# Kernel optimization log

Hardware: AMD Instinct MI355X
Metric: run time of the kernel (lower is better)

## Reference

```python
import jax, jax.numpy as jnp
import numpy as np

XI = 10.0
LAMBDA_SCALE = 1e-4
NUM_CLASSES = 13
KNOWN_NUM_CLASSES = 12  # all labels except 'unknown'
EPS = 1e-10
B, D = 262144, 512


def setup_inputs() -> dict:
    key = jax.random.key(0)
    k1, k2, k3, k4, k5 = jax.random.split(key, 5)
    logits = jax.random.normal(k1, (B, NUM_CLASSES), dtype=jnp.float32)
    true_y = jax.random.randint(k2, (B,), 0, NUM_CLASSES, dtype=jnp.int64)
    is_unknown = jax.random.randint(k3, (B,), 0, 2, dtype=jnp.int32).astype(bool)
    deep_features = jax.random.normal(k4, (B, D), dtype=jnp.float32)
    weights = jax.random.uniform(k5, (NUM_CLASSES,), dtype=jnp.float32, minval=0.5, maxval=2.0)
    return {"logits": logits, "true_y": true_y, "is_unknown": is_unknown,
            "deep_features": deep_features, "weights": weights}


def reference(logits, true_y, is_unknown, deep_features, weights):
    # softmax over classes, then log(softmax + eps) as in the original
    sm = jax.nn.softmax(logits, axis=1)                      # [B, C]
    log_sm = jnp.log(sm + EPS)                               # [B, C]
    feat_mag = jnp.linalg.norm(deep_features, axis=1)        # [B]

    # unknown branch: uniform log-loss over all classes + squared-magnitude penalty
    je_unknown = -(1.0 / KNOWN_NUM_CLASSES) * jnp.sum(log_sm, axis=1)
    pen_unknown = feat_mag ** 2
    jr_unknown = je_unknown + LAMBDA_SCALE * pen_unknown

    # known branch: NLL of true class + hinge-squared magnitude penalty
    je_known = -jnp.take_along_axis(log_sm, true_y[:, None], axis=1)[:, 0]
    pen_known = jnp.maximum(XI - feat_mag, 0.0) ** 2
    jr_known = je_known + LAMBDA_SCALE * pen_known

    jr = jnp.where(is_unknown, jr_unknown, jr_known)         # [B]
    w = weights[true_y]                                      # [B]
    loss = jnp.sum(w * jr) / jnp.sum(w)
    return loss
```

## Files before the change

kernel.cpp:

```cpp
#include <hip/hip_runtime.h>
#include <math.h>


typedef float f32x4 __attribute__((ext_vector_type(4)));

constexpr int   CLS  = 13;
constexpr float INV_KNOWN = 1.0f / 12.0f;
constexpr float LAM  = 1e-4f;
constexpr float XI   = 10.0f;

constexpr int BLOCK = 256;
constexpr int WPB   = BLOCK / 64;

template<int CTRL, int RMASK>
__device__ __forceinline__ float dpp_add(float v) {
    int t = __builtin_amdgcn_update_dpp(0, __builtin_bit_cast(int, v),
                                        CTRL, RMASK, 0xF, true);
    return v + __builtin_bit_cast(float, t);
}
__device__ __forceinline__ float read_lane_f(float v, int lane) {
    return __builtin_bit_cast(float,
        __builtin_amdgcn_readlane(__builtin_bit_cast(int, v), lane));
}

__global__ __launch_bounds__(256) void obj_main(
    const float*  __restrict__ logits,
    const int*    __restrict__ true_y,
    const int*    __restrict__ is_unknown,
    const f32x4*  __restrict__ feat,
    const float*  __restrict__ weights,
    double*       __restrict__ partials,
    int B)
{
    const int lane = threadIdx.x & 63;
    const int wid  = threadIdx.x >> 6;
    const int gw   = blockIdx.x * WPB + wid;
    const int tw   = gridDim.x * WPB;

    double num = 0.0, den = 0.0;

    int row = gw;
    f32x4 a = (f32x4)0.0f, b = (f32x4)0.0f;
    float x = 0.0f;
    if (row < B) {
        const f32x4* fr = feat + (size_t)row * 128;
        a = fr[lane];
        b = fr[lane + 64];
        if (lane < CLS) x = logits[(size_t)row * CLS + lane];
    }

    while (row < B) {
        const int nrow = row + tw;
        f32x4 na = (f32x4)0.0f, nb = (f32x4)0.0f;
        float nx = 0.0f;
        if (nrow < B) {
            const f32x4* fr = feat + (size_t)nrow * 128;
            na = fr[lane];
            nb = fr[lane + 64];
            if (lane < CLS) nx = logits[(size_t)nrow * CLS + lane];
        }

        float ss = fmaf(a.x, a.x, fmaf(a.y, a.y, fmaf(a.z, a.z, a.w * a.w)))
                 + fmaf(b.x, b.x, fmaf(b.y, b.y, fmaf(b.z, b.z, b.w * b.w)));
        const float e = (lane < CLS) ? __expf(x) : 0.0f;
        float S = e, sx = x;

        ss = dpp_add<0x111, 0xF>(ss);
        S  = dpp_add<0x111, 0xF>(S);
        sx = dpp_add<0x111, 0xF>(sx);
        ss = dpp_add<0x112, 0xF>(ss);
        S  = dpp_add<0x112, 0xF>(S);
        sx = dpp_add<0x112, 0xF>(sx);
        ss = dpp_add<0x114, 0xF>(ss);
        S  = dpp_add<0x114, 0xF>(S);
        sx = dpp_add<0x114, 0xF>(sx);
        ss = dpp_add<0x118, 0xF>(ss);
        S  = dpp_add<0x118, 0xF>(S);
        sx = dpp_add<0x118, 0xF>(sx);
        ss = dpp_add<0x142, 0xA>(ss);
        ss = dpp_add<0x143, 0xC>(ss);

        const int   ty    = true_y[row];
        const int   unk   = is_unknown[row];
        const float w     = weights[ty];
        const float ss_t  = read_lane_f(ss, 63);
        const float S_t   = read_lane_f(S,  15);
        const float sx_t  = read_lane_f(sx, 15);
        const float x_ty  = read_lane_f(x,  ty);
        const float logS  = __logf(S_t);
        const float mag   = sqrtf(ss_t);

        const float jr_u = fmaf(LAM, ss_t, -INV_KNOWN * (sx_t - (float)CLS * logS));
        const float dk   = fmaxf(XI - mag, 0.0f);
        const float jr_k = fmaf(LAM, dk * dk, logS - x_ty);
        const float jr   = unk ? jr_u : jr_k;

        num += (double)(w * jr);
        den += (double)w;

        row = nrow; a = na; b = nb; x = nx;
    }

    __shared__ double s_num[WPB], s_den[WPB];
    if (lane == 0) { s_num[wid] = num; s_den[wid] = den; }
    __syncthreads();
    if (threadIdx.x == 0) {
        double n = 0.0, d = 0.0;
        for (int i = 0; i < WPB; ++i) { n += s_num[i]; d += s_den[i]; }
        partials[blockIdx.x] = n;
        partials[gridDim.x + blockIdx.x] = d;
    }
}

__global__ __launch_bounds__(256) void obj_final(
    const double* __restrict__ partials, int nparts, float* __restrict__ out)
{
    const int lane = threadIdx.x & 63;
    const int wid  = threadIdx.x >> 6;
    double n = 0.0, d = 0.0;
    for (int i = threadIdx.x; i < nparts; i += blockDim.x) {
        n += partials[i];
        d += partials[nparts + i];
    }
    #pragma unroll
    for (int o = 32; o; o >>= 1) {
        n += __shfl_xor(n, o, 64);
        d += __shfl_xor(d, o, 64);
    }
    __shared__ double s_n[4], s_d[4];
    if (lane == 0) { s_n[wid] = n; s_d[wid] = d; }
    __syncthreads();
    if (threadIdx.x == 0) {
        double tn = 0.0, td = 0.0;
        for (int i = 0; i < 4; ++i) { tn += s_n[i]; td += s_d[i]; }
        out[0] = (float)(tn / td);
    }
}

extern "C" void kernel_launch(void* const* d_in, const int* in_sizes, int n_in,
                              void* d_out, int out_size, void* d_ws, size_t ws_size,
                              hipStream_t stream)
{
    const float*  logits     = (const float*)d_in[0];
    const int*    true_y     = (const int*)d_in[1];
    const int*    is_unknown = (const int*)d_in[2];
    const f32x4*  feat       = (const f32x4*)d_in[3];
    const float*  weights    = (const float*)d_in[4];
    float*        out        = (float*)d_out;
    const int B = in_sizes[1];

    double* partials = (double*)d_ws;
    constexpr int GRID = 2048;

    obj_main<<<GRID, BLOCK, 0, stream>>>(logits, true_y, is_unknown, feat,
                                         weights, partials, B);
    obj_final<<<1, 256, 0, stream>>>(partials, GRID, out);
}
```

Before: 101.7 us.

## Split softmax-NLL and feature-norm work into separate block groups

```diff
diff --git a/kernel.cpp b/kernel.cpp
--- a/kernel.cpp
+++ b/kernel.cpp
@@ -11,6 +11,8 @@
 
 constexpr int BLOCK = 256;
 constexpr int WPB   = BLOCK / 64;
+constexpr int NB_B  = 128;
+constexpr int NB_A  = 1920;
 
 template<int CTRL, int RMASK>
 __device__ __forceinline__ float dpp_add(float v) {
@@ -34,94 +36,116 @@
 {
     const int lane = threadIdx.x & 63;
     const int wid  = threadIdx.x >> 6;
-    const int gw   = blockIdx.x * WPB + wid;
-    const int tw   = gridDim.x * WPB;
 
-    double num = 0.0, den = 0.0;
+    if (blockIdx.x < NB_B) {
+        const int gwb = blockIdx.x * WPB + wid;
+        double numB = 0.0;
+        for (int it = 0; it < 8; ++it) {
+            const int r = (((gwb << 3) + it) << 6) | lane;
+            const float* lp = logits + (size_t)r * CLS;
+            float xv[CLS];
+            #pragma unroll
+            for (int c = 0; c < CLS; ++c) xv[c] = lp[c];
+            const int   ty  = true_y[r];
+            const int   unk = is_unknown[r];
+            const float w   = weights[ty];
 
-    int row = gw;
-    f32x4 a = (f32x4)0.0f, b = (f32x4)0.0f;
-    float x = 0.0f;
-    if (row < B) {
-        const f32x4* fr = feat + (size_t)row * 128;
-        a = fr[lane];
-        b = fr[lane + 64];
-        if (lane < CLS) x = logits[(size_t)row * CLS + lane];
-    }
+            float S = 0.0f, sx = 0.0f;
+            #pragma unroll
+            for (int c = 0; c < CLS; ++c) {
+                S  += __expf(xv[c]);
+                sx += xv[c];
+            }
+            const float logS = __logf(S);
+            float x_ty = xv[0];
+            #pragma unroll
+            for (int c = 1; c < CLS; ++c) x_ty = (ty == c) ? xv[c] : x_ty;
 
-    while (row < B) {
-        const int nrow = row + tw;
-        f32x4 na = (f32x4)0.0f, nb = (f32x4)0.0f;
-        float nx = 0.0f;
-        if (nrow < B) {
-            const f32x4* fr = feat + (size_t)nrow * 128;
-            na = fr[lane];
-            nb = fr[lane + 64];
-            if (lane < CLS) nx = logits[(size_t)nrow * CLS + lane];
+            const float je = unk ? (-INV_KNOWN * (sx - (float)CLS * logS))
+                                 : (logS - x_ty);
+            numB += (double)(w * je);
+        }
+        #pragma unroll
+        for (int o = 32; o; o >>= 1) numB += __shfl_xor(numB, o, 64);
+        __shared__ double s_b[WPB];
+        if (lane == 0) s_b[wid] = numB;
+        __syncthreads();
+        if (threadIdx.x == 0) {
+            double n = 0.0;
+            for (int i = 0; i < WPB; ++i) n += s_b[i];
+            partials[2 * NB_A + blockIdx.x] = n;
+        }
+    } else {
+        const int bidA = blockIdx.x - NB_B;
+        const int gw   = bidA * WPB + wid;
+        const int tw   = NB_A * WPB;
+
+        const float wreg = weights[lane < CLS ? lane : 0];
+
+        double num = 0.0, den = 0.0;
+        int row = gw;
+        f32x4 a = (f32x4)0.0f, b = (f32x4)0.0f;
+        if (row < B) {
+            const f32x4* fr = feat + (size_t)row * 128;
+            a = fr[lane];
+            b = fr[lane + 64];
         }
 
-        float ss = fmaf(a.x, a.x, fmaf(a.y, a.y, fmaf(a.z, a.z, a.w * a.w)))
-                 + fmaf(b.x, b.x, fmaf(b.y, b.y, fmaf(b.z, b.z, b.w * b.w)));
-        const float e = (lane < CLS) ? __expf(x) : 0.0f;
-        float S = e, sx = x;
+        while (row < B) {
+            const int nrow = row + tw;
+            f32x4 na = (f32x4)0.0f, nb = (f32x4)0.0f;
+            if (nrow < B) {
+                const f32x4* fr = feat + (size_t)nrow * 128;
+                na = fr[lane];
+                nb = fr[lane + 64];
+            }
 
-        ss = dpp_add<0x111, 0xF>(ss);
-        S  = dpp_add<0x111, 0xF>(S);
-        sx = dpp_add<0x111, 0xF>(sx);
-        ss = dpp_add<0x112, 0xF>(ss);
-        S  = dpp_add<0x112, 0xF>(S);
-        sx = dpp_add<0x112, 0xF>(sx);
-        ss = dpp_add<0x114, 0xF>(ss);
-        S  = dpp_add<0x114, 0xF>(S);
-        sx = dpp_add<0x114, 0xF>(sx);
-        ss = dpp_add<0x118, 0xF>(ss);
-        S  = dpp_add<0x118, 0xF>(S);
-        sx = dpp_add<0x118, 0xF>(sx);
-        ss = dpp_add<0x142, 0xA>(ss);
-        ss = dpp_add<0x143, 0xC>(ss);
+            float ss = fmaf(a.x, a.x, fmaf(a.y, a.y, fmaf(a.z, a.z, a.w * a.w)))
+                     + fmaf(b.x, b.x, fmaf(b.y, b.y, fmaf(b.z, b.z, b.w * b.w)));
+            ss = dpp_add<0x111, 0xF>(ss);
+            ss = dpp_add<0x112, 0xF>(ss);
+            ss = dpp_add<0x114, 0xF>(ss);
+            ss = dpp_add<0x118, 0xF>(ss);
+            ss = dpp_add<0x142, 0xA>(ss);
+            ss = dpp_add<0x143, 0xC>(ss);
 
-        const int   ty    = true_y[row];
-        const int   unk   = is_unknown[row];
-        const float w     = weights[ty];
-        const float ss_t  = read_lane_f(ss, 63);
-        const float S_t   = read_lane_f(S,  15);
-        const float sx_t  = read_lane_f(sx, 15);
-        const float x_ty  = read_lane_f(x,  ty);
-        const float logS  = __logf(S_t);
-        const float mag   = sqrtf(ss_t);
+            const int   ty   = true_y[row];
+            const int   unk  = is_unknown[row];
+            const float w    = read_lane_f(wreg, ty);
+            const float ss_t = read_lane_f(ss, 63);
+            const float mag  = sqrtf(ss_t);
+            const float dk   = fmaxf(XI - mag, 0.0f);
+            const float pen  = unk ? ss_t : dk * dk;
 
-        const float jr_u = fmaf(LAM, ss_t, -INV_KNOWN * (sx_t - (float)CLS * logS));
-        const float dk   = fmaxf(XI - mag, 0.0f);
-        const float jr_k = fmaf(LAM, dk * dk, logS - x_ty);
-        const float jr   = unk ? jr_u : jr_k;
+            num += (double)(w * (LAM * pen));
+            den += (double)w;
 
-        num += (double)(w * jr);
-        den += (double)w;
+            row = nrow; a = na; b = nb;
+        }
 
-        row = nrow; a = na; b = nb; x = nx;
-    }
-
-    __shared__ double s_num[WPB], s_den[WPB];
-    if (lane == 0) { s_num[wid] = num; s_den[wid] = den; }
-    __syncthreads();
-    if (threadIdx.x == 0) {
-        double n = 0.0, d = 0.0;
-        for (int i = 0; i < WPB; ++i) { n += s_num[i]; d += s_den[i]; }
-        partials[blockIdx.x] = n;
-        partials[gridDim.x + blockIdx.x] = d;
+        __shared__ double s_num[WPB], s_den[WPB];
+        if (lane == 0) { s_num[wid] = num; s_den[wid] = den; }
+        __syncthreads();
+        if (threadIdx.x == 0) {
+            double n = 0.0, d = 0.0;
+            for (int i = 0; i < WPB; ++i) { n += s_num[i]; d += s_den[i]; }
+            partials[bidA] = n;
+            partials[NB_A + bidA] = d;
+        }
     }
 }
 
 __global__ __launch_bounds__(256) void obj_final(
-    const double* __restrict__ partials, int nparts, float* __restrict__ out)
+    const double* __restrict__ partials, float* __restrict__ out)
 {
     const int lane = threadIdx.x & 63;
     const int wid  = threadIdx.x >> 6;
     double n = 0.0, d = 0.0;
-    for (int i = threadIdx.x; i < nparts; i += blockDim.x) {
+    for (int i = threadIdx.x; i < NB_A; i += blockDim.x) {
         n += partials[i];
-        d += partials[nparts + i];
+        d += partials[NB_A + i];
     }
+    if (threadIdx.x < NB_B) n += partials[2 * NB_A + threadIdx.x];
     #pragma unroll
     for (int o = 32; o; o >>= 1) {
         n += __shfl_xor(n, o, 64);
@@ -150,9 +174,8 @@
     const int B = in_sizes[1];
 
     double* partials = (double*)d_ws;
-    constexpr int GRID = 2048;
 
-    obj_main<<<GRID, BLOCK, 0, stream>>>(logits, true_y, is_unknown, feat,
-                                         weights, partials, B);
-    obj_final<<<1, 256, 0, stream>>>(partials, GRID, out);
+    obj_main<<<NB_A + NB_B, BLOCK, 0, stream>>>(logits, true_y, is_unknown,
+                                                feat, weights, partials, B);
+    obj_final<<<1, 256, 0, stream>>>(partials, out);
 }
```

Measured after the change: 106.9 us. 5.1% more time.
